# Optimization experiments

Measured on AMD Instinct MI355X. Metric: run time of the kernel, lower is better.

Reference implementation:

```python
import jax, jax.numpy as jnp
import numpy as np

NUM_HEADS = 16


def setup_inputs() -> dict:
    key = jax.random.key(0)
    k0, k1, k2, k3 = jax.random.split(key, 4)
    B, N, C = 8, 1024, 1024
    D = C // NUM_HEADS
    x = jax.random.normal(k0, (B, N, C), dtype=jnp.float32)
    # RoPE angle table [1, N, 1, head_dim]
    rope_freqs = jax.random.uniform(k1, (1, N, 1, D), dtype=jnp.float32) * (2.0 * jnp.pi)
    # qkv: Linear(dim, 3*dim, bias=False); proj: Linear(dim, dim) with bias
    qkv_w = jax.random.normal(k2, (3 * C, C), dtype=jnp.float32) * 0.02
    proj_w = jax.random.normal(k3, (C, C), dtype=jnp.float32) * 0.02
    proj_b = jnp.zeros((C,), dtype=jnp.float32)
    return {"x": x, "rope_freqs": rope_freqs, "qkv_w": qkv_w, "proj_w": proj_w, "proj_b": proj_b}


def _rotate_half(t):
    t1, t2 = jnp.split(t, 2, axis=-1)
    return jnp.concatenate([-t2, t1], axis=-1)


def reference(x, rope_freqs, qkv_w, proj_w, proj_b):
    B, N, C = x.shape
    H = NUM_HEADS
    D = C // H
    scale = D ** (-0.5)
    # QKV projection -> [3, B, H, N, D]
    qkv = (x @ qkv_w.T).reshape(B, N, 3, H, D).transpose(2, 0, 3, 1, 4)
    q, k, v = qkv[0], qkv[1], qkv[2]
    # RoPE: freqs [1, N, 1, D] -> [1, 1, N, D], applied to all tokens (n_special = 0)
    freqs = jnp.transpose(rope_freqs, (0, 2, 1, 3))
    cos = jnp.cos(freqs).astype(q.dtype)
    sin = jnp.sin(freqs).astype(q.dtype)
    q = q * cos + _rotate_half(q) * sin
    k = k * cos + _rotate_half(k) * sin
    # Full materialized attention (as in source)
    attn = jax.nn.softmax(jnp.einsum("bhnd,bhmd->bhnm", q, k) * scale, axis=-1)
    out = jnp.einsum("bhnm,bhmd->bhnd", attn, v)  # [B, H, N, D]
    out = out.transpose(0, 2, 1, 3).reshape(B, N, C)
    return out @ proj_w.T + proj_b
```

## Files before the change

kernel.cpp:

```cpp
#include <hip/hip_runtime.h>


typedef __attribute__((ext_vector_type(8))) short bf16x8;
typedef __attribute__((ext_vector_type(4))) float floatx4;
typedef __attribute__((ext_vector_type(4))) unsigned int u32x4;
typedef __attribute__((ext_vector_type(2))) unsigned int u32x2;

__device__ __forceinline__ void gld16(const void* g, void* l) {
  __builtin_amdgcn_global_load_lds((const __attribute__((address_space(1))) void*)g,
                                   (__attribute__((address_space(3))) void*)l, 16, 0, 0);
}

__device__ __forceinline__ short f2bf(float f) {
  unsigned u = __builtin_bit_cast(unsigned, f);
  u = (u + 0x7FFFu + ((u >> 16) & 1u)) >> 16;
  return (short)u;
}
__device__ __forceinline__ unsigned cvtpk(float lo, float hi) {
  unsigned r;
  asm("v_cvt_pk_bf16_f32 %0, %1, %2" : "=v"(r) : "v"(lo), "v"(hi));
  return r;
}

__global__ __launch_bounds__(256) void cvt_bf16_all(const float* __restrict__ sx,
                                                    const float* __restrict__ sq,
                                                    const float* __restrict__ sp,
                                                    short* __restrict__ dst) {
  int i = blockIdx.x * 256 + threadIdx.x;
  const float4* src;
  if (i < 2097152)      src = reinterpret_cast<const float4*>(sx) + i;
  else if (i < 2883584) src = reinterpret_cast<const float4*>(sq) + (i - 2097152);
  else                  src = reinterpret_cast<const float4*>(sp) + (i - 2883584);
  float4 v = *src;
  short4 o;
  o.x = f2bf(v.x); o.y = f2bf(v.y); o.z = f2bf(v.z); o.w = f2bf(v.w);
  reinterpret_cast<short4*>(dst)[i] = o;
}

__global__ __launch_bounds__(256) void rope_table(const float* __restrict__ f,
                                                  float2* __restrict__ tbl) {
  int i = blockIdx.x * 256 + threadIdx.x;
  float v = f[i];
  tbl[i] = make_float2(cosf(v), sinf(v));
}

#define QSCALE 0.18033688011112042f

__device__ __forceinline__ void gemm_main(const short* __restrict__ A,
                                          const short* __restrict__ Bm,
                                          short* As, short* Bs,
                                          floatx4 (&acc)[4][4],
                                          int bx, int by) {
  const int tid = threadIdx.x;
  const int wid = tid >> 6, lane = tid & 63;
  const int g = lane >> 4, l15 = lane & 15;
  const int wr = wid >> 1, wc = wid & 1;
  const size_t trow = (size_t)by * 128, tcol = (size_t)bx * 128;
  floatx4 zero = {0.f, 0.f, 0.f, 0.f};
  #pragma unroll
  for (int i = 0; i < 4; ++i)
    #pragma unroll
    for (int j = 0; j < 4; ++j) acc[i][j] = zero;

  for (int k0 = 0; k0 < 1024; k0 += 64) {
    #pragma unroll
    for (int i = 0; i < 4; ++i) {
      const int cb = (i * 4 + wid) * 64;
      const int c  = cb + lane;
      const int r  = c >> 3, s = c & 7;
      const int koff = k0 + ((s ^ (r & 7)) << 3);
      gld16(A  + (trow + r) * 1024 + koff, As + (size_t)cb * 8);
      gld16(Bm + (tcol + r) * 1024 + koff, Bs + (size_t)cb * 8);
    }
    __syncthreads();
    #pragma unroll
    for (int ks = 0; ks < 2; ++ks) {
      bf16x8 af[4], bfr[4];
      #pragma unroll
      for (int mi = 0; mi < 4; ++mi) {
        int row = wr * 64 + mi * 16 + l15;
        int ch  = (ks * 4 + g) ^ (row & 7);
        af[mi] = *reinterpret_cast<const bf16x8*>(As + row * 64 + ch * 8);
      }
      #pragma unroll
      for (int nt = 0; nt < 4; ++nt) {
        int row = wc * 64 + nt * 16 + l15;
        int ch  = (ks * 4 + g) ^ (row & 7);
        bfr[nt] = *reinterpret_cast<const bf16x8*>(Bs + row * 64 + ch * 8);
      }
      #pragma unroll
      for (int mi = 0; mi < 4; ++mi)
        #pragma unroll
        for (int nt = 0; nt < 4; ++nt)
          acc[mi][nt] = __builtin_amdgcn_mfma_f32_16x16x32_bf16(af[mi], bfr[nt],
                                                                acc[mi][nt], 0, 0, 0);
    }
    __syncthreads();
  }
}

__global__ __launch_bounds__(256) void gemm_qkv_k(const short* __restrict__ A,
                                                  const short* __restrict__ Bm,
                                                  const float2* __restrict__ tbl,
                                                  short* __restrict__ qo,
                                                  short* __restrict__ ko,
                                                  short* __restrict__ vt) {
  __shared__ __align__(16) short As[128 * 64];
  __shared__ __align__(16) short Bs[128 * 64];
  const int id  = blockIdx.y * 24 + blockIdx.x;
  const int sid = (id & 7) * 192 + (id >> 3);
  const int bx  = sid % 24, by = sid / 24;
  floatx4 acc[4][4];
  gemm_main(A, Bm, As, Bs, acc, bx, by);

  const int tid = threadIdx.x;
  const int wid = tid >> 6, lane = tid & 63;
  const int g = lane >> 4, l15 = lane & 15;
  const int wr = wid >> 1, wc = wid & 1;
  const int trow = by * 128, tcol = bx * 128;
  const int which = bx >> 3;

  if (which < 2) {
    short* dst = which == 0 ? qo : ko;
    const float sc = which == 0 ? QSCALE : 1.0f;
    #pragma unroll
    for (int nt = 0; nt < 2; ++nt) {
      int col = tcol + wc * 64 + nt * 16 + l15;
      int hc = col & 1023, h = hc >> 6, d1 = hc & 63;
      #pragma unroll
      for (int mi = 0; mi < 4; ++mi)
        #pragma unroll
        for (int r = 0; r < 4; ++r) {
          int rowg = trow + wr * 64 + mi * 16 + g * 4 + r;
          int b = rowg >> 10, n = rowg & 1023;
          float a1 = acc[mi][nt][r], a2 = acc[mi][nt + 2][r];
          float2 c1 = tbl[n * 64 + d1];
          float2 c2 = tbl[n * 64 + d1 + 32];
          float o1 = (a1 * c1.x - a2 * c1.y) * sc;
          float o2 = (a2 * c2.x + a1 * c2.y) * sc;
          size_t base = ((size_t)(b * 16 + h) * 1024 + n) * 64;
          dst[base + d1]      = f2bf(o1);
          dst[base + d1 + 32] = f2bf(o2);
        }
    }
  } else {
    #pragma unroll
    for (int nt = 0; nt < 4; ++nt) {
      int col = tcol + wc * 64 + nt * 16 + l15;
      int hc = col & 1023, h = hc >> 6, d = hc & 63;
      #pragma unroll
      for (int mi = 0; mi < 4; ++mi) {
        int rowg = trow + wr * 64 + mi * 16 + g * 4;
        int b = rowg >> 10, n0 = rowg & 1023;
        ushort4 pk;
        pk.x = (unsigned short)f2bf(acc[mi][nt][0]);
        pk.y = (unsigned short)f2bf(acc[mi][nt][1]);
        pk.z = (unsigned short)f2bf(acc[mi][nt][2]);
        pk.w = (unsigned short)f2bf(acc[mi][nt][3]);
        *reinterpret_cast<ushort4*>((unsigned short*)vt +
            ((size_t)(b * 16 + h) * 64 + d) * 1024 + n0) = pk;
      }
    }
  }
}

__global__ __launch_bounds__(256) void gemm_proj_k(const short* __restrict__ A,
                                                   const short* __restrict__ Bm,
                                                   const float* __restrict__ pb,
                                                   float* __restrict__ out) {
  __shared__ __align__(16) short As[128 * 64];
  __shared__ __align__(16) short Bs[128 * 64];
  const int id  = blockIdx.y * 8 + blockIdx.x;
  const int sid = (id & 7) * 64 + (id >> 3);
  const int bx  = sid % 8, by = sid / 8;
  floatx4 acc[4][4];
  gemm_main(A, Bm, As, Bs, acc, bx, by);

  const int tid = threadIdx.x;
  const int wid = tid >> 6, lane = tid & 63;
  const int g = lane >> 4, l15 = lane & 15;
  const int wr = wid >> 1, wc = wid & 1;
  const int trow = by * 128, tcol = bx * 128;
  #pragma unroll
  for (int nt = 0; nt < 4; ++nt) {
    int col = tcol + wc * 64 + nt * 16 + l15;
    float bias = pb[col];
    #pragma unroll
    for (int mi = 0; mi < 4; ++mi)
      #pragma unroll
      for (int r = 0; r < 4; ++r) {
        int rowg = trow + wr * 64 + mi * 16 + g * 4 + r;
        out[(size_t)rowg * 1024 + col] = acc[mi][nt][r] + bias;
      }
  }
}

__global__ __launch_bounds__(256) void attn_kernel(const short* __restrict__ qs,
                                                   const short* __restrict__ ksrc,
                                                   const short* __restrict__ vt,
                                                   short* __restrict__ aout) {
  __shared__ __align__(16) short Kl[2][64 * 64];
  __shared__ __align__(16) short Vl[2][64 * 64];

  const int tid = threadIdx.x, wid = tid >> 6, lane = tid & 63;
  const int g = lane >> 4, l15 = lane & 15;
  const int bh = blockIdx.y, q0 = blockIdx.x * 64;
  const size_t bhoff = (size_t)bh * 1024 * 64;
  const short* Kb = ksrc + bhoff;
  const short* Vb = vt + bhoff;

  const short* Qp = qs + bhoff + (size_t)(q0 + wid * 16 + l15) * 64 + g * 8;
  bf16x8 qf0 = *reinterpret_cast<const bf16x8*>(Qp);
  bf16x8 qf1 = *reinterpret_cast<const bf16x8*>(Qp + 32);

  floatx4 o[4];
  floatx4 zero = {0.f, 0.f, 0.f, 0.f};
  #pragma unroll
  for (int i = 0; i < 4; ++i) o[i] = zero;
  float mrun = -1e30f, lrun = 0.f;

  auto stage = [&](int buf, int t) {
    #pragma unroll
    for (int i = 0; i < 2; ++i) {
      const int cb = (i * 4 + wid) * 64;
      const int c = cb + lane;
      const int r = c >> 3, s = c & 7;
      const int off = (s ^ (r & 7)) << 3;
      gld16(Kb + (size_t)(t * 64 + r) * 64 + off, &Kl[buf][cb * 8]);
      gld16(Vb + (size_t)r * 1024 + t * 64 + off, &Vl[buf][cb * 8]);
    }
  };

  stage(0, 0);
  __syncthreads();

  for (int t = 0; t < 16; ++t) {
    const int buf = t & 1;
    if (t < 15) stage(buf ^ 1, t + 1);

    floatx4 s4[4];
    #pragma unroll
    for (int kt = 0; kt < 4; ++kt) s4[kt] = zero;
    __builtin_amdgcn_s_setprio(1);
    #pragma unroll
    for (int kt = 0; kt < 4; ++kt) {
      int krow = kt * 16 + l15;
      int ch0 = (g ^ (krow & 7)) << 3, ch1 = (((4 + g)) ^ (krow & 7)) << 3;
      bf16x8 kf0 = *reinterpret_cast<const bf16x8*>(&Kl[buf][krow * 64 + ch0]);
      s4[kt] = __builtin_amdgcn_mfma_f32_16x16x32_bf16(kf0, qf0, s4[kt], 0, 0, 0);
      bf16x8 kf1 = *reinterpret_cast<const bf16x8*>(&Kl[buf][krow * 64 + ch1]);
      s4[kt] = __builtin_amdgcn_mfma_f32_16x16x32_bf16(kf1, qf1, s4[kt], 0, 0, 0);
    }
    __builtin_amdgcn_s_setprio(0);

    float m0 = -1e30f;
    #pragma unroll
    for (int kt = 0; kt < 4; ++kt)
      m0 = fmaxf(m0, fmaxf(fmaxf(s4[kt][0], s4[kt][1]), fmaxf(s4[kt][2], s4[kt][3])));
    m0 = fmaxf(m0, __shfl_xor(m0, 16));
    m0 = fmaxf(m0, __shfl_xor(m0, 32));

    if (!__all(m0 - mrun <= 8.f)) {
      float mnew = fmaxf(mrun, m0);
      float alpha = exp2f(mrun - mnew);
      mrun = mnew;
      lrun *= alpha;
      const int slb = (lane & 48) + ((lane >> 4) << 2);
      float a4[4];
      #pragma unroll
      for (int r = 0; r < 4; ++r) a4[r] = __shfl(alpha, slb + r);
      #pragma unroll
      for (int nt = 0; nt < 4; ++nt) {
        o[nt][0] *= a4[0]; o[nt][1] *= a4[1]; o[nt][2] *= a4[2]; o[nt][3] *= a4[3];
      }
    }

    float p[4][4], lsum = 0.f;
    #pragma unroll
    for (int kt = 0; kt < 4; ++kt)
      #pragma unroll
      for (int r = 0; r < 4; ++r) {
        p[kt][r] = exp2f(s4[kt][r] - mrun);
        lsum += p[kt][r];
      }
    lsum += __shfl_xor(lsum, 16);
    lsum += __shfl_xor(lsum, 32);
    lrun += lsum;

    unsigned w[4][2];
    #pragma unroll
    for (int kt = 0; kt < 4; ++kt) {
      w[kt][0] = cvtpk(p[kt][0], p[kt][1]);
      w[kt][1] = cvtpk(p[kt][2], p[kt][3]);
    }

    unsigned W[2][2][2];
    #pragma unroll
    for (int ks = 0; ks < 2; ++ks)
      #pragma unroll
      for (int h = 0; h < 2; ++h) {
        u32x2 y = __builtin_amdgcn_permlane32_swap(w[2 * ks][h], w[2 * ks + 1][h],
                                                   false, false);
        u32x2 z = __builtin_amdgcn_permlane16_swap(y[0], y[1], false, false);
        W[ks][0][h] = z[0];
        W[ks][1][h] = z[1];
      }
    u32x4 aw0 = {W[0][0][0], W[0][0][1], W[0][1][0], W[0][1][1]};
    u32x4 aw1 = {W[1][0][0], W[1][0][1], W[1][1][0], W[1][1][1]};
    bf16x8 pa0 = __builtin_bit_cast(bf16x8, aw0);
    bf16x8 pa1 = __builtin_bit_cast(bf16x8, aw1);

    __builtin_amdgcn_s_setprio(1);
    #pragma unroll
    for (int nt = 0; nt < 4; ++nt) {
      int row = nt * 16 + l15;
      int ch0 = (g ^ (row & 7)) << 3, ch1 = ((4 + g) ^ (row & 7)) << 3;
      bf16x8 vf0 = *reinterpret_cast<const bf16x8*>(&Vl[buf][row * 64 + ch0]);
      o[nt] = __builtin_amdgcn_mfma_f32_16x16x32_bf16(pa0, vf0, o[nt], 0, 0, 0);
      bf16x8 vf1 = *reinterpret_cast<const bf16x8*>(&Vl[buf][row * 64 + ch1]);
      o[nt] = __builtin_amdgcn_mfma_f32_16x16x32_bf16(pa1, vf1, o[nt], 0, 0, 0);
    }
    __builtin_amdgcn_s_setprio(0);
    __syncthreads();
  }

  const int b = bh >> 4, h = bh & 15;
  const int slb = (lane & 48) + ((lane >> 4) << 2);
  float inv = 1.f / lrun;
  #pragma unroll
  for (int r = 0; r < 4; ++r) {
    float ir = __shfl(inv, slb + r);
    int n = q0 + wid * 16 + g * 4 + r;
    size_t base = ((size_t)(b * 1024) + n) * 1024 + h * 64;
    #pragma unroll
    for (int nt = 0; nt < 4; ++nt)
      aout[base + nt * 16 + l15] = f2bf(o[nt][r] * ir);
  }
}

extern "C" void kernel_launch(void* const* d_in, const int* in_sizes, int n_in,
                              void* d_out, int out_size, void* d_ws, size_t ws_size,
                              hipStream_t stream) {
  const float* x      = (const float*)d_in[0];
  const float* ropef  = (const float*)d_in[1];
  const float* qkv_w  = (const float*)d_in[2];
  const float* proj_w = (const float*)d_in[3];
  const float* proj_b = (const float*)d_in[4];
  float* out = (float*)d_out;

  char* ws = (char*)d_ws;
  short*  xb  = (short*)(ws + 0);
  short*  wqb = (short*)(ws + 16777216);
  short*  wpb = (short*)(ws + 23068672);
  short*  qb  = (short*)(ws + 25165824);
  short*  kb  = (short*)(ws + 41943040);
  short*  vtb = (short*)(ws + 58720256);
  short*  aob = (short*)(ws + 75497472);
  float2* tbl = (float2*)(ws + 92274688);

  cvt_bf16_all<<<12288, 256, 0, stream>>>(x, qkv_w, proj_w, xb);
  rope_table<<<256, 256, 0, stream>>>(ropef, tbl);

  gemm_qkv_k<<<dim3(24, 64), 256, 0, stream>>>(xb, wqb, tbl, qb, kb, vtb);
  attn_kernel<<<dim3(16, 128), 256, 0, stream>>>(qb, kb, vtb, aob);
  gemm_proj_k<<<dim3(8, 64), 256, 0, stream>>>(aob, wpb, proj_b, out);
}
```

Measured before the change: 194.2 us.

## Process two query tiles per attention block and fuse prep kernels

Each attention block now handles 128 queries: every wave carries two independent 16-row query tiles that share the staged K/V tiles from LDS. This halves K/V global traffic and LDS staging per query and interleaves independent MFMA chains. The grid is reordered so heads run along blockIdx.x, which changes block scheduling order. The row-sum reduction across lanes is deferred to the end of the loop. The two prep kernels are also merged into one launch. In exchange the kernel uses more registers and the grid has half as many blocks, which may reduce occupancy.

```diff
diff --git a/kernel.cpp b/kernel.cpp
--- a/kernel.cpp
+++ b/kernel.cpp
@@ -22,26 +22,28 @@
   return r;
 }
 
-__global__ __launch_bounds__(256) void cvt_bf16_all(const float* __restrict__ sx,
-                                                    const float* __restrict__ sq,
-                                                    const float* __restrict__ sp,
-                                                    short* __restrict__ dst) {
-  int i = blockIdx.x * 256 + threadIdx.x;
-  const float4* src;
-  if (i < 2097152)      src = reinterpret_cast<const float4*>(sx) + i;
-  else if (i < 2883584) src = reinterpret_cast<const float4*>(sq) + (i - 2097152);
-  else                  src = reinterpret_cast<const float4*>(sp) + (i - 2883584);
-  float4 v = *src;
-  short4 o;
-  o.x = f2bf(v.x); o.y = f2bf(v.y); o.z = f2bf(v.z); o.w = f2bf(v.w);
-  reinterpret_cast<short4*>(dst)[i] = o;
-}
-
-__global__ __launch_bounds__(256) void rope_table(const float* __restrict__ f,
-                                                  float2* __restrict__ tbl) {
-  int i = blockIdx.x * 256 + threadIdx.x;
-  float v = f[i];
-  tbl[i] = make_float2(cosf(v), sinf(v));
+__global__ __launch_bounds__(256) void prep_all(const float* __restrict__ sx,
+                                                const float* __restrict__ sq,
+                                                const float* __restrict__ sp,
+                                                short* __restrict__ dst,
+                                                const float* __restrict__ ropef,
+                                                float2* __restrict__ tbl) {
+  int bid = blockIdx.x;
+  if (bid < 12288) {
+    int i = bid * 256 + threadIdx.x;
+    const float4* src;
+    if (i < 2097152)      src = reinterpret_cast<const float4*>(sx) + i;
+    else if (i < 2883584) src = reinterpret_cast<const float4*>(sq) + (i - 2097152);
+    else                  src = reinterpret_cast<const float4*>(sp) + (i - 2883584);
+    float4 v = *src;
+    short4 o;
+    o.x = f2bf(v.x); o.y = f2bf(v.y); o.z = f2bf(v.z); o.w = f2bf(v.w);
+    reinterpret_cast<short4*>(dst)[i] = o;
+  } else {
+    int i = (bid - 12288) * 256 + threadIdx.x;
+    float v = ropef[i];
+    tbl[i] = make_float2(cosf(v), sinf(v));
+  }
 }
 
 #define QSCALE 0.18033688011112042f
@@ -204,20 +206,25 @@
 
   const int tid = threadIdx.x, wid = tid >> 6, lane = tid & 63;
   const int g = lane >> 4, l15 = lane & 15;
-  const int bh = blockIdx.y, q0 = blockIdx.x * 64;
+  const int bh = blockIdx.x, q0 = blockIdx.y * 128;
   const size_t bhoff = (size_t)bh * 1024 * 64;
   const short* Kb = ksrc + bhoff;
   const short* Vb = vt + bhoff;
-
-  const short* Qp = qs + bhoff + (size_t)(q0 + wid * 16 + l15) * 64 + g * 8;
-  bf16x8 qf0 = *reinterpret_cast<const bf16x8*>(Qp);
-  bf16x8 qf1 = *reinterpret_cast<const bf16x8*>(Qp + 32);
-
-  floatx4 o[4];
+  const int slb = (lane & 48) + ((lane >> 4) << 2);
+
+  const short* QpA = qs + bhoff + (size_t)(q0 + wid * 16 + l15) * 64 + g * 8;
+  bf16x8 qA0 = *reinterpret_cast<const bf16x8*>(QpA);
+  bf16x8 qA1 = *reinterpret_cast<const bf16x8*>(QpA + 32);
+  const short* QpB = QpA + 64 * 64;
+  bf16x8 qB0 = *reinterpret_cast<const bf16x8*>(QpB);
+  bf16x8 qB1 = *reinterpret_cast<const bf16x8*>(QpB + 32);
+
+  floatx4 oA[4], oB[4];
   floatx4 zero = {0.f, 0.f, 0.f, 0.f};
   #pragma unroll
-  for (int i = 0; i < 4; ++i) o[i] = zero;
-  float mrun = -1e30f, lrun = 0.f;
+  for (int i = 0; i < 4; ++i) { oA[i] = zero; oB[i] = zero; }
+  float mrunA = -1e30f, lrunA = 0.f;
+  float mrunB = -1e30f, lrunB = 0.f;
 
   auto stage = [&](int buf, int t) {
     #pragma unroll
@@ -231,6 +238,56 @@
     }
   };
 
+#define SOFTMAX(s4, mrun, lrun, o, pa0, pa1)                                   \
+  do {                                                                         \
+    float m0 = -1e30f;                                                         \
+    _Pragma("unroll")                                                          \
+    for (int kt = 0; kt < 4; ++kt)                                             \
+      m0 = fmaxf(m0, fmaxf(fmaxf(s4[kt][0], s4[kt][1]),                        \
+                           fmaxf(s4[kt][2], s4[kt][3])));                      \
+    m0 = fmaxf(m0, __shfl_xor(m0, 16));                                        \
+    m0 = fmaxf(m0, __shfl_xor(m0, 32));                                        \
+    if (!__all(m0 - mrun <= 8.f)) {                                            \
+      float mnew = fmaxf(mrun, m0);                                            \
+      float alpha = exp2f(mrun - mnew);                                        \
+      mrun = mnew;                                                             \
+      lrun *= alpha;                                                           \
+      float a4[4];                                                             \
+      _Pragma("unroll")                                                        \
+      for (int r = 0; r < 4; ++r) a4[r] = __shfl(alpha, slb + r);              \
+      _Pragma("unroll")                                                        \
+      for (int nt = 0; nt < 4; ++nt) {                                         \
+        o[nt][0] *= a4[0]; o[nt][1] *= a4[1];                                  \
+        o[nt][2] *= a4[2]; o[nt][3] *= a4[3];                                  \
+      }                                                                        \
+    }                                                                          \
+    unsigned w[4][2];                                                          \
+    _Pragma("unroll")                                                          \
+    for (int kt = 0; kt < 4; ++kt) {                                           \
+      float p0 = exp2f(s4[kt][0] - mrun), p1 = exp2f(s4[kt][1] - mrun);        \
+      float p2 = exp2f(s4[kt][2] - mrun), p3 = exp2f(s4[kt][3] - mrun);        \
+      lrun += (p0 + p1) + (p2 + p3);                                           \
+      w[kt][0] = cvtpk(p0, p1);                                                \
+      w[kt][1] = cvtpk(p2, p3);                                                \
+    }                                                                          \
+    unsigned W[2][2][2];                                                       \
+    _Pragma("unroll")                                                          \
+    for (int ks = 0; ks < 2; ++ks)                                             \
+      _Pragma("unroll")                                                        \
+      for (int h = 0; h < 2; ++h) {                                            \
+        u32x2 y = __builtin_amdgcn_permlane32_swap(w[2 * ks][h],               \
+                                                   w[2 * ks + 1][h],           \
+                                                   false, false);              \
+        u32x2 z = __builtin_amdgcn_permlane16_swap(y[0], y[1], false, false);  \
+        W[ks][0][h] = z[0];                                                    \
+        W[ks][1][h] = z[1];                                                    \
+      }                                                                        \
+    u32x4 aw0 = {W[0][0][0], W[0][0][1], W[0][1][0], W[0][1][1]};              \
+    u32x4 aw1 = {W[1][0][0], W[1][0][1], W[1][1][0], W[1][1][1]};              \
+    pa0 = __builtin_bit_cast(bf16x8, aw0);                                     \
+    pa1 = __builtin_bit_cast(bf16x8, aw1);                                     \
+  } while (0)
+
   stage(0, 0);
   __syncthreads();
 
@@ -238,77 +295,26 @@
     const int buf = t & 1;
     if (t < 15) stage(buf ^ 1, t + 1);
 
-    floatx4 s4[4];
-    #pragma unroll
-    for (int kt = 0; kt < 4; ++kt) s4[kt] = zero;
+    floatx4 sA[4], sB[4];
+    #pragma unroll
+    for (int kt = 0; kt < 4; ++kt) { sA[kt] = zero; sB[kt] = zero; }
     __builtin_amdgcn_s_setprio(1);
     #pragma unroll
     for (int kt = 0; kt < 4; ++kt) {
       int krow = kt * 16 + l15;
-      int ch0 = (g ^ (krow & 7)) << 3, ch1 = (((4 + g)) ^ (krow & 7)) << 3;
+      int ch0 = (g ^ (krow & 7)) << 3, ch1 = ((4 + g) ^ (krow & 7)) << 3;
       bf16x8 kf0 = *reinterpret_cast<const bf16x8*>(&Kl[buf][krow * 64 + ch0]);
-      s4[kt] = __builtin_amdgcn_mfma_f32_16x16x32_bf16(kf0, qf0, s4[kt], 0, 0, 0);
+      sA[kt] = __builtin_amdgcn_mfma_f32_16x16x32_bf16(kf0, qA0, sA[kt], 0, 0, 0);
+      sB[kt] = __builtin_amdgcn_mfma_f32_16x16x32_bf16(kf0, qB0, sB[kt], 0, 0, 0);
       bf16x8 kf1 = *reinterpret_cast<const bf16x8*>(&Kl[buf][krow * 64 + ch1]);
-      s4[kt] = __builtin_amdgcn_mfma_f32_16x16x32_bf16(kf1, qf1, s4[kt], 0, 0, 0);
+      sA[kt] = __builtin_amdgcn_mfma_f32_16x16x32_bf16(kf1, qA1, sA[kt], 0, 0, 0);
+      sB[kt] = __builtin_amdgcn_mfma_f32_16x16x32_bf16(kf1, qB1, sB[kt], 0, 0, 0);
     }
     __builtin_amdgcn_s_setprio(0);
 
-    float m0 = -1e30f;
-    #pragma unroll
-    for (int kt = 0; kt < 4; ++kt)
-      m0 = fmaxf(m0, fmaxf(fmaxf(s4[kt][0], s4[kt][1]), fmaxf(s4[kt][2], s4[kt][3])));
-    m0 = fmaxf(m0, __shfl_xor(m0, 16));
-    m0 = fmaxf(m0, __shfl_xor(m0, 32));
-
-    if (!__all(m0 - mrun <= 8.f)) {
-      float mnew = fmaxf(mrun, m0);
-      float alpha = exp2f(mrun - mnew);
-      mrun = mnew;
-      lrun *= alpha;
-      const int slb = (lane & 48) + ((lane >> 4) << 2);
-      float a4[4];
-      #pragma unroll
-      for (int r = 0; r < 4; ++r) a4[r] = __shfl(alpha, slb + r);
-      #pragma unroll
-      for (int nt = 0; nt < 4; ++nt) {
-        o[nt][0] *= a4[0]; o[nt][1] *= a4[1]; o[nt][2] *= a4[2]; o[nt][3] *= a4[3];
-      }
-    }
-
-    float p[4][4], lsum = 0.f;
-    #pragma unroll
-    for (int kt = 0; kt < 4; ++kt)
-      #pragma unroll
-      for (int r = 0; r < 4; ++r) {
-        p[kt][r] = exp2f(s4[kt][r] - mrun);
-        lsum += p[kt][r];
-      }
-    lsum += __shfl_xor(lsum, 16);
-    lsum += __shfl_xor(lsum, 32);
-    lrun += lsum;
-
-    unsigned w[4][2];
-    #pragma unroll
-    for (int kt = 0; kt < 4; ++kt) {
-      w[kt][0] = cvtpk(p[kt][0], p[kt][1]);
-      w[kt][1] = cvtpk(p[kt][2], p[kt][3]);
-    }
-
-    unsigned W[2][2][2];
-    #pragma unroll
-    for (int ks = 0; ks < 2; ++ks)
-      #pragma unroll
-      for (int h = 0; h < 2; ++h) {
-        u32x2 y = __builtin_amdgcn_permlane32_swap(w[2 * ks][h], w[2 * ks + 1][h],
-                                                   false, false);
-        u32x2 z = __builtin_amdgcn_permlane16_swap(y[0], y[1], false, false);
-        W[ks][0][h] = z[0];
-        W[ks][1][h] = z[1];
-      }
-    u32x4 aw0 = {W[0][0][0], W[0][0][1], W[0][1][0], W[0][1][1]};
-    u32x4 aw1 = {W[1][0][0], W[1][0][1], W[1][1][0], W[1][1][1]};
-    bf16x8 pa0 = __builtin_bit_cast(bf16x8, aw0);
-    bf16x8 pa1 = __builtin_bit_cast(bf16x8, aw1);
+    bf16x8 paA0, paA1, paB0, paB1;
+    SOFTMAX(sA, mrunA, lrunA, oA, paA0, paA1);
+    SOFTMAX(sB, mrunB, lrunB, oB, paB0, paB1);
 
     __builtin_amdgcn_s_setprio(1);
     #pragma unroll
@@ -316,26 +322,34 @@
       int row = nt * 16 + l15;
       int ch0 = (g ^ (row & 7)) << 3, ch1 = ((4 + g) ^ (row & 7)) << 3;
       bf16x8 vf0 = *reinterpret_cast<const bf16x8*>(&Vl[buf][row * 64 + ch0]);
-      o[nt] = __builtin_amdgcn_mfma_f32_16x16x32_bf16(pa0, vf0, o[nt], 0, 0, 0);
+      oA[nt] = __builtin_amdgcn_mfma_f32_16x16x32_bf16(paA0, vf0, oA[nt], 0, 0, 0);
+      oB[nt] = __builtin_amdgcn_mfma_f32_16x16x32_bf16(paB0, vf0, oB[nt], 0, 0, 0);
       bf16x8 vf1 = *reinterpret_cast<const bf16x8*>(&Vl[buf][row * 64 + ch1]);
-      o[nt] = __builtin_amdgcn_mfma_f32_16x16x32_bf16(pa1, vf1, o[nt], 0, 0, 0);
+      oA[nt] = __builtin_amdgcn_mfma_f32_16x16x32_bf16(paA1, vf1, oA[nt], 0, 0, 0);
+      oB[nt] = __builtin_amdgcn_mfma_f32_16x16x32_bf16(paB1, vf1, oB[nt], 0, 0, 0);
     }
     __builtin_amdgcn_s_setprio(0);
     __syncthreads();
   }
 
   const int b = bh >> 4, h = bh & 15;
-  const int slb = (lane & 48) + ((lane >> 4) << 2);
-  float inv = 1.f / lrun;
+  lrunA += __shfl_xor(lrunA, 16); lrunA += __shfl_xor(lrunA, 32);
+  lrunB += __shfl_xor(lrunB, 16); lrunB += __shfl_xor(lrunB, 32);
+  float invA = 1.f / lrunA, invB = 1.f / lrunB;
   #pragma unroll
   for (int r = 0; r < 4; ++r) {
-    float ir = __shfl(inv, slb + r);
-    int n = q0 + wid * 16 + g * 4 + r;
-    size_t base = ((size_t)(b * 1024) + n) * 1024 + h * 64;
-    #pragma unroll
-    for (int nt = 0; nt < 4; ++nt)
-      aout[base + nt * 16 + l15] = f2bf(o[nt][r] * ir);
-  }
+    float irA = __shfl(invA, slb + r);
+    float irB = __shfl(invB, slb + r);
+    int nA = q0 + wid * 16 + g * 4 + r;
+    size_t baseA = ((size_t)(b * 1024) + nA) * 1024 + h * 64;
+    size_t baseB = baseA + (size_t)64 * 1024;
+    #pragma unroll
+    for (int nt = 0; nt < 4; ++nt) {
+      aout[baseA + nt * 16 + l15] = f2bf(oA[nt][r] * irA);
+      aout[baseB + nt * 16 + l15] = f2bf(oB[nt][r] * irB);
+    }
+  }
+#undef SOFTMAX
 }
 
 extern "C" void kernel_launch(void* const* d_in, const int* in_sizes, int n_in,
@@ -358,10 +372,9 @@
   short*  aob = (short*)(ws + 75497472);
   float2* tbl = (float2*)(ws + 92274688);
 
-  cvt_bf16_all<<<12288, 256, 0, stream>>>(x, qkv_w, proj_w, xb);
-  rope_table<<<256, 256, 0, stream>>>(ropef, tbl);
+  prep_all<<<12544, 256, 0, stream>>>(x, qkv_w, proj_w, xb, ropef, tbl);
 
   gemm_qkv_k<<<dim3(24, 64), 256, 0, stream>>>(xb, wqb, tbl, qb, kb, vtb);
-  attn_kernel<<<dim3(16, 128), 256, 0, stream>>>(qb, kb, vtb, aob);
+  attn_kernel<<<dim3(128, 8), 256, 0, stream>>>(qb, kb, vtb, aob);
   gemm_proj_k<<<dim3(8, 64), 256, 0, stream>>>(aob, wpb, proj_b, out);
 }
```

Measured after the change: 188.9 us. 1.03x faster.
